# Kernel tuning notes

Hardware: AMD Instinct MI355X
Metric: run time of the kernel (lower is better)

## Reference

```python
import jax, jax.numpy as jnp
import numpy as np

N, F, H, L, O, E = 20000, 128, 128, 4, 64, 640000
NEG_SLOPE = 0.2  # PyG GATConv default


def setup_inputs() -> dict:
    key = jax.random.key(0)
    ks = jax.random.split(key, 8)
    x = jax.random.normal(ks[0], (N, F), dtype=jnp.float32)
    edge_index = jax.random.randint(ks[1], (2, E), 0, N, dtype=jnp.int64)
    sc = 1.0 / np.sqrt(F)
    Ws = jax.random.normal(ks[2], (L, F, H), dtype=jnp.float32) * sc
    att_src = jax.random.normal(ks[3], (L, H), dtype=jnp.float32) * sc
    att_dst = jax.random.normal(ks[4], (L, H), dtype=jnp.float32) * sc
    biases = jnp.zeros((L, H), dtype=jnp.float32)
    W_out = jax.random.normal(ks[5], (H, O), dtype=jnp.float32) * (1.0 / np.sqrt(H))
    b_out = jnp.zeros((O,), dtype=jnp.float32)
    return {"x": x, "edge_index": edge_index, "Ws": Ws, "att_src": att_src,
            "att_dst": att_dst, "biases": biases, "W_out": W_out, "b_out": b_out}


def _gat_conv(h, src, dst, W, a_s, a_d, b):
    # h: [N, F_in]; single-head GATConv (PyG semantics)
    z = h @ W                                   # [N, H]
    alpha_s = z @ a_s                           # [N]
    alpha_d = z @ a_d                           # [N]
    logits = jax.nn.leaky_relu(alpha_s[src] + alpha_d[dst], negative_slope=NEG_SLOPE)  # [E']
    # segment-softmax over edges grouped by destination node
    m = jax.ops.segment_max(logits, dst, num_segments=N)
    p = jnp.exp(logits - m[dst])
    s = jax.ops.segment_sum(p, dst, num_segments=N)
    alpha = p / (s[dst] + 1e-16)                # [E']
    out = jax.ops.segment_sum(alpha[:, None] * z[src], dst, num_segments=N)  # [N, H]
    return out + b


def reference(x, edge_index, Ws, att_src, att_dst, biases, W_out, b_out):
    # add self-loops once (PyG GATConv default add_self_loops=True)
    loop = jnp.arange(N, dtype=edge_index.dtype)
    src = jnp.concatenate([edge_index[0], loop])
    dst = jnp.concatenate([edge_index[1], loop])
    h = x
    for l in range(L):
        h = _gat_conv(h, src, dst, Ws[l], att_src[l], att_dst[l], biases[l])
        h = jax.nn.relu(h)  # Dropout is identity at eval
    return h @ W_out + b_out  # [N, O]
```

## Files before the change

kernel.cpp:

```cpp
#include <hip/hip_runtime.h>

#define NN 20000
#define FF 128
#define HH 128
#define LL 4
#define OO 64
#define EE 640000
#define NEG 0.2f
#define NB ((NN + 255) / 256)
#define NTILES (NN / 16)
#define ZS 132

typedef short bf16x8 __attribute__((ext_vector_type(8)));
typedef float f32x4 __attribute__((ext_vector_type(4)));

__device__ inline ushort f2bf(float f) {
    uint u = __float_as_uint(f);
    return (ushort)((u + 0x7fffu + ((u >> 16) & 1u)) >> 16);
}


__global__ void k_init_counters(int* __restrict__ counters) {
    int i = blockIdx.x * 256 + threadIdx.x;
    if (i < NN) counters[i] = 1;
}

__global__ void k_hist(const int* __restrict__ dst, int* __restrict__ counters) {
    int e = blockIdx.x * 256 + threadIdx.x;
    if (e < EE) atomicAdd(&counters[dst[e]], 1);
}

__global__ void k_partial(const int* __restrict__ counters, int* __restrict__ partials) {
    __shared__ int ws[4];
    int t = threadIdx.x;
    int i = blockIdx.x * 256 + t;
    int c = (i < NN) ? counters[i] : 0;
    #pragma unroll
    for (int off = 32; off; off >>= 1) c += __shfl_xor(c, off);
    if ((t & 63) == 0) ws[t >> 6] = c;
    __syncthreads();
    if (t == 0) partials[blockIdx.x] = ws[0] + ws[1] + ws[2] + ws[3];
}

__global__ void k_scan_small(const int* __restrict__ partials, int* __restrict__ offsets) {
    __shared__ int sp[128];
    int t = threadIdx.x;
    int v = (t < NB) ? partials[t] : 0;
    sp[t] = v;
    __syncthreads();
    for (int off = 1; off < 128; off <<= 1) {
        int u = (t >= off) ? sp[t - off] : 0;
        __syncthreads();
        sp[t] += u;
        __syncthreads();
    }
    if (t < NB) offsets[t] = sp[t] - v;
}

__global__ void k_apply(const int* __restrict__ counters, const int* __restrict__ offsets,
                        int* __restrict__ row_off, int* __restrict__ cursor,
                        int* __restrict__ src_sorted) {
    __shared__ int sc[256];
    int t = threadIdx.x;
    int i = blockIdx.x * 256 + t;
    int c = (i < NN) ? counters[i] : 0;
    sc[t] = c;
    __syncthreads();
    for (int off = 1; off < 256; off <<= 1) {
        int u = (t >= off) ? sc[t - off] : 0;
        __syncthreads();
        sc[t] += u;
        __syncthreads();
    }
    int incl = sc[t];
    int base = offsets[blockIdx.x];
    if (i < NN) {
        int excl = base + incl - c;
        row_off[i] = excl;
        cursor[i] = excl + 1;
        src_sorted[excl] = i;
        if (i == NN - 1) row_off[NN] = base + incl;
    }
}

__global__ void k_scatter(const int* __restrict__ src, const int* __restrict__ dst,
                          int* __restrict__ cursor, int* __restrict__ src_sorted) {
    int e = blockIdx.x * 256 + threadIdx.x;
    if (e < EE) {
        int p = atomicAdd(&cursor[dst[e]], 1);
        src_sorted[p] = src[e];
    }
}


__global__ void k_convw(const float* __restrict__ Ws, const float* __restrict__ Wout,
                        ushort* __restrict__ wh, ushort* __restrict__ wl) {
    int idx = blockIdx.x * 256 + threadIdx.x;
    const int per_l = HH * 128;
    float v;
    if (idx < LL * per_l) {
        int l = idx / per_l, rem = idx % per_l;
        int n = rem >> 7, k = rem & 127;
        v = Ws[(size_t)l * 128 * HH + (size_t)k * HH + n];
    } else {
        int j = idx - LL * per_l;
        if (j >= OO * 128) return;
        int n = j >> 7, k = j & 127;
        v = Wout[(size_t)k * OO + n];
    }
    ushort h = f2bf(v);
    float hf = __uint_as_float((uint)h << 16);
    wh[idx] = h;
    wl[idx] = f2bf(v - hf);
}


__global__ void k_wa(const float* __restrict__ Ws, const float* __restrict__ attS,
                     const float* __restrict__ attD, float* __restrict__ wa) {
    int t = blockIdx.x * 256 + threadIdx.x;
    if (t >= LL * 256) return;
    int l = t >> 8, rem = t & 255, which = rem >> 7, k = rem & 127;
    const float* wrow = Ws + (size_t)l * 128 * HH + (size_t)k * HH;
    const float* av = (which ? attD : attS) + l * HH;
    float s = 0.f;
    #pragma unroll 4
    for (int n = 0; n < HH; n++) s += wrow[n] * av[n];
    wa[l * 256 + which * 128 + k] = s;
}


__device__ inline void do_agg(const float* __restrict__ zin, const int* __restrict__ row_off,
                              const int* __restrict__ srcs, const float* __restrict__ bias,
                              float (*h)[132], int node0, int wid, int l64) {
    int g = l64 >> 5, cl = l64 & 31;
    const float4* zb = (const float4*)zin;
    #pragma unroll 1
    for (int i = 0; i < 2; i++) {
        int node = node0 + wid * 2 + i;
        int beg = row_off[node], end = row_off[node + 1];
        float adn = zin[(size_t)node * ZS + 1];
        float lself = zin[(size_t)node * ZS] + adn;
        float mx = (lself >= 0.f) ? lself : NEG * lself;

        float4 acc = make_float4(0.f, 0.f, 0.f, 0.f);
        float s = 0.f;
        for (int e = beg + g; e < end; e += 16) {
            int e1 = e + 2, e2 = e + 4, e3 = e + 6, e4 = e + 8, e5 = e + 10, e6 = e + 12, e7 = e + 14;
            int lim = end - 1;
            int i1 = min(e1, lim), i2 = min(e2, lim), i3 = min(e3, lim);
            int i4 = min(e4, lim), i5 = min(e5, lim), i6 = min(e6, lim), i7 = min(e7, lim);
            int s0 = srcs[e], s1 = srcs[i1], s2 = srcs[i2], s3 = srcs[i3];
            int s4 = srcs[i4], s5 = srcs[i5], s6 = srcs[i6], s7 = srcs[i7];
            float l0 = zin[(size_t)s0 * ZS] + adn, l1 = zin[(size_t)s1 * ZS] + adn;
            float l2 = zin[(size_t)s2 * ZS] + adn, l3 = zin[(size_t)s3 * ZS] + adn;
            float l4 = zin[(size_t)s4 * ZS] + adn, l5 = zin[(size_t)s5 * ZS] + adn;
            float l6 = zin[(size_t)s6 * ZS] + adn, l7 = zin[(size_t)s7 * ZS] + adn;
            l0 = (l0 >= 0.f) ? l0 : NEG * l0;  l1 = (l1 >= 0.f) ? l1 : NEG * l1;
            l2 = (l2 >= 0.f) ? l2 : NEG * l2;  l3 = (l3 >= 0.f) ? l3 : NEG * l3;
            l4 = (l4 >= 0.f) ? l4 : NEG * l4;  l5 = (l5 >= 0.f) ? l5 : NEG * l5;
            l6 = (l6 >= 0.f) ? l6 : NEG * l6;  l7 = (l7 >= 0.f) ? l7 : NEG * l7;
            float4 z0 = zb[(size_t)s0 * 33 + 1 + cl];
            float4 z1 = zb[(size_t)s1 * 33 + 1 + cl];
            float4 z2 = zb[(size_t)s2 * 33 + 1 + cl];
            float4 z3 = zb[(size_t)s3 * 33 + 1 + cl];
            float4 z4 = zb[(size_t)s4 * 33 + 1 + cl];
            float4 z5 = zb[(size_t)s5 * 33 + 1 + cl];
            float4 z6 = zb[(size_t)s6 * 33 + 1 + cl];
            float4 z7 = zb[(size_t)s7 * 33 + 1 + cl];
            float p0 = __expf(l0 - mx);
            float p1 = (e1 < end) ? __expf(l1 - mx) : 0.f;
            float p2 = (e2 < end) ? __expf(l2 - mx) : 0.f;
            float p3 = (e3 < end) ? __expf(l3 - mx) : 0.f;
            float p4 = (e4 < end) ? __expf(l4 - mx) : 0.f;
            float p5 = (e5 < end) ? __expf(l5 - mx) : 0.f;
            float p6 = (e6 < end) ? __expf(l6 - mx) : 0.f;
            float p7 = (e7 < end) ? __expf(l7 - mx) : 0.f;
            s += ((p0 + p1) + (p2 + p3)) + ((p4 + p5) + (p6 + p7));
            acc.x += (p0 * z0.x + p1 * z1.x + p2 * z2.x + p3 * z3.x)
                   + (p4 * z4.x + p5 * z5.x + p6 * z6.x + p7 * z7.x);
            acc.y += (p0 * z0.y + p1 * z1.y + p2 * z2.y + p3 * z3.y)
                   + (p4 * z4.y + p5 * z5.y + p6 * z6.y + p7 * z7.y);
            acc.z += (p0 * z0.z + p1 * z1.z + p2 * z2.z + p3 * z3.z)
                   + (p4 * z4.z + p5 * z5.z + p6 * z6.z + p7 * z7.z);
            acc.w += (p0 * z0.w + p1 * z1.w + p2 * z2.w + p3 * z3.w)
                   + (p4 * z4.w + p5 * z5.w + p6 * z6.w + p7 * z7.w);
        }
        acc.x += __shfl_xor(acc.x, 32);
        acc.y += __shfl_xor(acc.y, 32);
        acc.z += __shfl_xor(acc.z, 32);
        acc.w += __shfl_xor(acc.w, 32);
        s     += __shfl_xor(s, 32);
        if (g == 0) {
            float inv = 1.f / (s + 1e-16f);
            float4 b = ((const float4*)bias)[cl];
            int lrow = wid * 2 + i;
            h[lrow][cl * 4 + 0] = fmaxf(acc.x * inv + b.x, 0.f);
            h[lrow][cl * 4 + 1] = fmaxf(acc.y * inv + b.y, 0.f);
            h[lrow][cl * 4 + 2] = fmaxf(acc.z * inv + b.z, 0.f);
            h[lrow][cl * 4 + 3] = fmaxf(acc.w * inv + b.w, 0.f);
        }
    }
}

template <int NCOL, bool BIAS, bool ALPHAS, bool PACKED>
__device__ inline void do_gemm(const float (*h)[132], const ushort* __restrict__ wh,
                               const ushort* __restrict__ wl, const float* __restrict__ bias,
                               float* __restrict__ C, const float* __restrict__ wa,
                               int row0, int wid, int l64) {
    constexpr int CT = NCOL / 16;
    if (wid >= CT) return;
    int lr = l64 & 15, lg = l64 >> 4;
    int col0 = wid * 16;

    f32x4 af0[4], af1[4];
    #pragma unroll
    for (int s = 0; s < 4; s++) {
        af0[s] = *(const f32x4*)&h[lr][s * 32 + lg * 8];
        af1[s] = *(const f32x4*)&h[lr][s * 32 + lg * 8 + 4];
    }
    bf16x8 ah[4], al[4];
    #pragma unroll
    for (int s = 0; s < 4; s++) {
        #pragma unroll
        for (int j = 0; j < 8; j++) {
            float v = (j < 4) ? af0[s][j] : af1[s][j - 4];
            ushort hb = f2bf(v);
            float hf = __uint_as_float((uint)hb << 16);
            ah[s][j] = (short)hb;
            al[s][j] = (short)f2bf(v - hf);
        }
    }

    f32x4 acc = {0.f, 0.f, 0.f, 0.f};
    #pragma unroll
    for (int s = 0; s < 4; s++) {
        int woff = (col0 + lr) * 128 + s * 32 + lg * 8;
        bf16x8 bh = *(const bf16x8*)(wh + woff);
        bf16x8 bl = *(const bf16x8*)(wl + woff);
        acc = __builtin_amdgcn_mfma_f32_16x16x32_bf16(ah[s], bh, acc, 0, 0, 0);
        acc = __builtin_amdgcn_mfma_f32_16x16x32_bf16(ah[s], bl, acc, 0, 0, 0);
        acc = __builtin_amdgcn_mfma_f32_16x16x32_bf16(al[s], bh, acc, 0, 0, 0);
    }

    int orow = lg * 4;
    #pragma unroll
    for (int r = 0; r < 4; r++) {
        float v = acc[r];
        if (BIAS) v += bias[col0 + lr];
        if (PACKED)
            C[(size_t)(row0 + orow + r) * ZS + 4 + col0 + lr] = v;
        else
            C[(size_t)(row0 + orow + r) * NCOL + col0 + lr] = v;
    }

    if constexpr (ALPHAS) {
        if (wid == 0) {
            float ps = 0.f, pd = 0.f;
            #pragma unroll
            for (int s = 0; s < 4; s++) {
                #pragma unroll
                for (int j = 0; j < 8; j++) {
                    float v = (j < 4) ? af0[s][j] : af1[s][j - 4];
                    int k = s * 32 + lg * 8 + j;
                    ps += v * wa[k];
                    pd += v * wa[128 + k];
                }
            }
            ps += __shfl_xor(ps, 16);  pd += __shfl_xor(pd, 16);
            ps += __shfl_xor(ps, 32);  pd += __shfl_xor(pd, 32);
            if (lg == 0) {
                C[(size_t)(row0 + lr) * ZS + 0] = ps;
                C[(size_t)(row0 + lr) * ZS + 1] = pd;
            }
        }
    }
}


__global__ __launch_bounds__(512)
void k_layer0(const float* __restrict__ x, const ushort* __restrict__ wh,
              const ushort* __restrict__ wl, const float* __restrict__ wa,
              float* __restrict__ z) {
    __shared__ float h[16][132];
    int t = threadIdx.x, wid = t >> 6, l64 = t & 63;
    int row0 = blockIdx.x * 16;
    {
        int r = t >> 5, c4 = (t & 31) << 2;
        *(float4*)&h[r][c4] = *(const float4*)&x[(size_t)(row0 + r) * 128 + c4];
    }
    __syncthreads();
    do_gemm<HH, false, true, true>(h, wh, wl, nullptr, z, wa, row0, wid, l64);
}

template <int NCOL, bool BIAS, bool ALPHAS, bool PACKED>
__global__ __launch_bounds__(512)
void k_layer(const float* __restrict__ zin, const int* __restrict__ row_off,
             const int* __restrict__ srcs, const float* __restrict__ abias,
             const ushort* __restrict__ wh, const ushort* __restrict__ wl,
             const float* __restrict__ cbias, const float* __restrict__ wa,
             float* __restrict__ zout) {
    __shared__ float h[16][132];
    int t = threadIdx.x, wid = t >> 6, l64 = t & 63;
    int row0 = blockIdx.x * 16;
    do_agg(zin, row_off, srcs, abias, h, row0, wid, l64);
    __syncthreads();
    do_gemm<NCOL, BIAS, ALPHAS, PACKED>(h, wh, wl, cbias, zout, wa, row0, wid, l64);
}


extern "C" void kernel_launch(void* const* d_in, const int* in_sizes, int n_in,
                              void* d_out, int out_size, void* d_ws, size_t ws_size,
                              hipStream_t stream) {
    const float* x      = (const float*)d_in[0];
    const int*   ei     = (const int*)d_in[1];
    const float* Ws     = (const float*)d_in[2];
    const float* attS   = (const float*)d_in[3];
    const float* attD   = (const float*)d_in[4];
    const float* biases = (const float*)d_in[5];
    const float* W_out  = (const float*)d_in[6];
    const float* b_out  = (const float*)d_in[7];
    float* out = (float*)d_out;

    const int* srcp = ei;
    const int* dstp = ei + EE;

    char* w = (char*)d_ws;
    auto take = [&](size_t bytes) {
        char* p = w;
        w += (bytes + 15) & ~(size_t)15;
        return p;
    };
    float*  za         = (float*)take((size_t)NN * ZS * 4);
    float*  zbv        = (float*)take((size_t)NN * ZS * 4);
    int*    counters   = (int*)take((size_t)NN * 4);
    int*    row_off    = (int*)take((size_t)(NN + 1) * 4);
    int*    cursor     = (int*)take((size_t)NN * 4);
    int*    src_sorted = (int*)take((size_t)(EE + NN) * 4);
    int*    partials   = (int*)take((size_t)NB * 4);
    int*    offsets    = (int*)take((size_t)NB * 4);
    const int WTOT = LL * HH * 128 + OO * 128;
    ushort* whbuf      = (ushort*)take((size_t)WTOT * 2);
    ushort* wlbuf      = (ushort*)take((size_t)WTOT * 2);
    float*  wabuf      = (float*)take((size_t)LL * 256 * 4);

    k_init_counters<<<(NN + 255) / 256, 256, 0, stream>>>(counters);
    k_hist<<<(EE + 255) / 256, 256, 0, stream>>>(dstp, counters);
    k_partial<<<NB, 256, 0, stream>>>(counters, partials);
    k_scan_small<<<1, 128, 0, stream>>>(partials, offsets);
    k_apply<<<NB, 256, 0, stream>>>(counters, offsets, row_off, cursor, src_sorted);
    k_scatter<<<(EE + 255) / 256, 256, 0, stream>>>(srcp, dstp, cursor, src_sorted);
    k_convw<<<(WTOT + 255) / 256, 256, 0, stream>>>(Ws, W_out, whbuf, wlbuf);
    k_wa<<<(LL * 256 + 255) / 256, 256, 0, stream>>>(Ws, attS, attD, wabuf);

    k_layer0<<<NTILES, 512, 0, stream>>>(x, whbuf, wlbuf, wabuf, za);

    k_layer<HH, false, true, true><<<NTILES, 512, 0, stream>>>(
        za, row_off, src_sorted, biases + 0 * HH,
        whbuf + (size_t)1 * HH * 128, wlbuf + (size_t)1 * HH * 128,
        nullptr, wabuf + 1 * 256, zbv);
    k_layer<HH, false, true, true><<<NTILES, 512, 0, stream>>>(
        zbv, row_off, src_sorted, biases + 1 * HH,
        whbuf + (size_t)2 * HH * 128, wlbuf + (size_t)2 * HH * 128,
        nullptr, wabuf + 2 * 256, za);
    k_layer<HH, false, true, true><<<NTILES, 512, 0, stream>>>(
        za, row_off, src_sorted, biases + 2 * HH,
        whbuf + (size_t)3 * HH * 128, wlbuf + (size_t)3 * HH * 128,
        nullptr, wabuf + 3 * 256, zbv);

    k_layer<OO, true, false, false><<<NTILES, 512, 0, stream>>>(
        zbv, row_off, src_sorted, biases + 3 * HH,
        whbuf + (size_t)LL * HH * 128, wlbuf + (size_t)LL * HH * 128,
        b_out, nullptr, out);
}
```

Before: 361.0 us.

## Split node features into column-quarter planes and separate attention scalar arrays

Stores the per-node feature matrix as four 32-column planes of size NN×32, and moves the source and destination attention scalars into their own dense arrays. The aggregation now loops over the four planes, with 8 lanes covering 32 columns and 8 edge groups per wave. The goal is for each 128B gathered row segment to be reused from a smaller cache working set. The cost is that the edge list and source indices are re-read four times per node, each pass has less unrolling to overlap memory latency, and more shuffle reductions are needed.

```diff
diff --git a/kernel.cpp b/kernel.cpp
--- a/kernel.cpp
+++ b/kernel.cpp
@@ -9,7 +9,6 @@
 #define NEG 0.2f
 #define NB ((NN + 255) / 256)
 #define NTILES (NN / 16)
-#define ZS 132
 
 typedef short bf16x8 __attribute__((ext_vector_type(8)));
 typedef float f32x4 __attribute__((ext_vector_type(4)));
@@ -129,83 +128,77 @@
 }
 
 
-__device__ inline void do_agg(const float* __restrict__ zin, const int* __restrict__ row_off,
+__device__ inline void do_agg(const float* __restrict__ zq, const float* __restrict__ asv,
+                              const float* __restrict__ adv, const int* __restrict__ row_off,
                               const int* __restrict__ srcs, const float* __restrict__ bias,
                               float (*h)[132], int node0, int wid, int l64) {
-    int g = l64 >> 5, cl = l64 & 31;
-    const float4* zb = (const float4*)zin;
+    int c4 = l64 & 7, ep = l64 >> 3;
     #pragma unroll 1
     for (int i = 0; i < 2; i++) {
         int node = node0 + wid * 2 + i;
         int beg = row_off[node], end = row_off[node + 1];
-        float adn = zin[(size_t)node * ZS + 1];
-        float lself = zin[(size_t)node * ZS] + adn;
+        float adn = adv[node];
+        float lself = asv[node] + adn;
         float mx = (lself >= 0.f) ? lself : NEG * lself;
-
-        float4 acc = make_float4(0.f, 0.f, 0.f, 0.f);
-        float s = 0.f;
-        for (int e = beg + g; e < end; e += 16) {
-            int e1 = e + 2, e2 = e + 4, e3 = e + 6, e4 = e + 8, e5 = e + 10, e6 = e + 12, e7 = e + 14;
-            int lim = end - 1;
-            int i1 = min(e1, lim), i2 = min(e2, lim), i3 = min(e3, lim);
-            int i4 = min(e4, lim), i5 = min(e5, lim), i6 = min(e6, lim), i7 = min(e7, lim);
-            int s0 = srcs[e], s1 = srcs[i1], s2 = srcs[i2], s3 = srcs[i3];
-            int s4 = srcs[i4], s5 = srcs[i5], s6 = srcs[i6], s7 = srcs[i7];
-            float l0 = zin[(size_t)s0 * ZS] + adn, l1 = zin[(size_t)s1 * ZS] + adn;
-            float l2 = zin[(size_t)s2 * ZS] + adn, l3 = zin[(size_t)s3 * ZS] + adn;
-            float l4 = zin[(size_t)s4 * ZS] + adn, l5 = zin[(size_t)s5 * ZS] + adn;
-            float l6 = zin[(size_t)s6 * ZS] + adn, l7 = zin[(size_t)s7 * ZS] + adn;
-            l0 = (l0 >= 0.f) ? l0 : NEG * l0;  l1 = (l1 >= 0.f) ? l1 : NEG * l1;
-            l2 = (l2 >= 0.f) ? l2 : NEG * l2;  l3 = (l3 >= 0.f) ? l3 : NEG * l3;
-            l4 = (l4 >= 0.f) ? l4 : NEG * l4;  l5 = (l5 >= 0.f) ? l5 : NEG * l5;
-            l6 = (l6 >= 0.f) ? l6 : NEG * l6;  l7 = (l7 >= 0.f) ? l7 : NEG * l7;
-            float4 z0 = zb[(size_t)s0 * 33 + 1 + cl];
-            float4 z1 = zb[(size_t)s1 * 33 + 1 + cl];
-            float4 z2 = zb[(size_t)s2 * 33 + 1 + cl];
-            float4 z3 = zb[(size_t)s3 * 33 + 1 + cl];
-            float4 z4 = zb[(size_t)s4 * 33 + 1 + cl];
-            float4 z5 = zb[(size_t)s5 * 33 + 1 + cl];
-            float4 z6 = zb[(size_t)s6 * 33 + 1 + cl];
-            float4 z7 = zb[(size_t)s7 * 33 + 1 + cl];
-            float p0 = __expf(l0 - mx);
-            float p1 = (e1 < end) ? __expf(l1 - mx) : 0.f;
-            float p2 = (e2 < end) ? __expf(l2 - mx) : 0.f;
-            float p3 = (e3 < end) ? __expf(l3 - mx) : 0.f;
-            float p4 = (e4 < end) ? __expf(l4 - mx) : 0.f;
-            float p5 = (e5 < end) ? __expf(l5 - mx) : 0.f;
-            float p6 = (e6 < end) ? __expf(l6 - mx) : 0.f;
-            float p7 = (e7 < end) ? __expf(l7 - mx) : 0.f;
-            s += ((p0 + p1) + (p2 + p3)) + ((p4 + p5) + (p6 + p7));
-            acc.x += (p0 * z0.x + p1 * z1.x + p2 * z2.x + p3 * z3.x)
-                   + (p4 * z4.x + p5 * z5.x + p6 * z6.x + p7 * z7.x);
-            acc.y += (p0 * z0.y + p1 * z1.y + p2 * z2.y + p3 * z3.y)
-                   + (p4 * z4.y + p5 * z5.y + p6 * z6.y + p7 * z7.y);
-            acc.z += (p0 * z0.z + p1 * z1.z + p2 * z2.z + p3 * z3.z)
-                   + (p4 * z4.z + p5 * z5.z + p6 * z6.z + p7 * z7.z);
-            acc.w += (p0 * z0.w + p1 * z1.w + p2 * z2.w + p3 * z3.w)
-                   + (p4 * z4.w + p5 * z5.w + p6 * z6.w + p7 * z7.w);
+        int lrow = wid * 2 + i;
+
+        #pragma unroll 1
+        for (int q = 0; q < 4; q++) {
+            const float* qbase = zq + (size_t)q * NN * 32;
+            float4 acc = make_float4(0.f, 0.f, 0.f, 0.f);
+            float s = 0.f;
+            for (int e = beg + ep; e < end; e += 16) {
+                int lim = end - 1;
+                int i1 = min(e + 8, lim);
+                int s0 = srcs[e], s1 = srcs[i1];
+                float l0 = asv[s0] + adn, l1 = asv[s1] + adn;
+                l0 = (l0 >= 0.f) ? l0 : NEG * l0;
+                l1 = (l1 >= 0.f) ? l1 : NEG * l1;
+                float4 z0 = *(const float4*)(qbase + (size_t)s0 * 32 + c4 * 4);
+                float4 z1 = *(const float4*)(qbase + (size_t)s1 * 32 + c4 * 4);
+                float p0 = __expf(l0 - mx);
+                float p1 = (e + 8 < end) ? __expf(l1 - mx) : 0.f;
+                s += p0 + p1;
+                acc.x += p0 * z0.x + p1 * z1.x;
+                acc.y += p0 * z0.y + p1 * z1.y;
+                acc.z += p0 * z0.z + p1 * z1.z;
+                acc.w += p0 * z0.w + p1 * z1.w;
+            }
+            acc.x += __shfl_xor(acc.x, 8);
+            acc.y += __shfl_xor(acc.y, 8);
+            acc.z += __shfl_xor(acc.z, 8);
+            acc.w += __shfl_xor(acc.w, 8);
+            s     += __shfl_xor(s, 8);
+            acc.x += __shfl_xor(acc.x, 16);
+            acc.y += __shfl_xor(acc.y, 16);
+            acc.z += __shfl_xor(acc.z, 16);
+            acc.w += __shfl_xor(acc.w, 16);
+            s     += __shfl_xor(s, 16);
+            acc.x += __shfl_xor(acc.x, 32);
+            acc.y += __shfl_xor(acc.y, 32);
+            acc.z += __shfl_xor(acc.z, 32);
+            acc.w += __shfl_xor(acc.w, 32);
+            s     += __shfl_xor(s, 32);
+            if (ep == 0) {
+                float inv = 1.f / (s + 1e-16f);
+                float4 b = ((const float4*)bias)[q * 8 + c4];
+                float4 o;
+                o.x = fmaxf(acc.x * inv + b.x, 0.f);
+                o.y = fmaxf(acc.y * inv + b.y, 0.f);
+                o.z = fmaxf(acc.z * inv + b.z, 0.f);
+                o.w = fmaxf(acc.w * inv + b.w, 0.f);
+                *(float4*)&h[lrow][q * 32 + c4 * 4] = o;
+            }
         }
-        acc.x += __shfl_xor(acc.x, 32);
-        acc.y += __shfl_xor(acc.y, 32);
-        acc.z += __shfl_xor(acc.z, 32);
-        acc.w += __shfl_xor(acc.w, 32);
-        s     += __shfl_xor(s, 32);
-        if (g == 0) {
-            float inv = 1.f / (s + 1e-16f);
-            float4 b = ((const float4*)bias)[cl];
-            int lrow = wid * 2 + i;
-            h[lrow][cl * 4 + 0] = fmaxf(acc.x * inv + b.x, 0.f);
-            h[lrow][cl * 4 + 1] = fmaxf(acc.y * inv + b.y, 0.f);
-            h[lrow][cl * 4 + 2] = fmaxf(acc.z * inv + b.z, 0.f);
-            h[lrow][cl * 4 + 3] = fmaxf(acc.w * inv + b.w, 0.f);
-        }
-    }
-}
+    }
+}
+
 
 template <int NCOL, bool BIAS, bool ALPHAS, bool PACKED>
 __device__ inline void do_gemm(const float (*h)[132], const ushort* __restrict__ wh,
                                const ushort* __restrict__ wl, const float* __restrict__ bias,
                                float* __restrict__ C, const float* __restrict__ wa,
+                               float* __restrict__ as_o, float* __restrict__ ad_o,
                                int row0, int wid, int l64) {
     constexpr int CT = NCOL / 16;
     if (wid >= CT) return;
@@ -243,14 +236,15 @@
     }
 
     int orow = lg * 4;
+    int c = col0 + lr;
     #pragma unroll
     for (int r = 0; r < 4; r++) {
         float v = acc[r];
-        if (BIAS) v += bias[col0 + lr];
+        if (BIAS) v += bias[c];
         if (PACKED)
-            C[(size_t)(row0 + orow + r) * ZS + 4 + col0 + lr] = v;
+            C[((size_t)(c >> 5) * NN + (row0 + orow + r)) * 32 + (c & 31)] = v;
         else
-            C[(size_t)(row0 + orow + r) * NCOL + col0 + lr] = v;
+            C[(size_t)(row0 + orow + r) * NCOL + c] = v;
     }
 
     if constexpr (ALPHAS) {
@@ -269,8 +263,8 @@
             ps += __shfl_xor(ps, 16);  pd += __shfl_xor(pd, 16);
             ps += __shfl_xor(ps, 32);  pd += __shfl_xor(pd, 32);
             if (lg == 0) {
-                C[(size_t)(row0 + lr) * ZS + 0] = ps;
-                C[(size_t)(row0 + lr) * ZS + 1] = pd;
+                as_o[row0 + lr] = ps;
+                ad_o[row0 + lr] = pd;
             }
         }
     }
@@ -280,7 +274,7 @@
 __global__ __launch_bounds__(512)
 void k_layer0(const float* __restrict__ x, const ushort* __restrict__ wh,
               const ushort* __restrict__ wl, const float* __restrict__ wa,
-              float* __restrict__ z) {
+              float* __restrict__ zq, float* __restrict__ as_o, float* __restrict__ ad_o) {
     __shared__ float h[16][132];
     int t = threadIdx.x, wid = t >> 6, l64 = t & 63;
     int row0 = blockIdx.x * 16;
@@ -289,22 +283,24 @@
         *(float4*)&h[r][c4] = *(const float4*)&x[(size_t)(row0 + r) * 128 + c4];
     }
     __syncthreads();
-    do_gemm<HH, false, true, true>(h, wh, wl, nullptr, z, wa, row0, wid, l64);
+    do_gemm<HH, false, true, true>(h, wh, wl, nullptr, zq, wa, as_o, ad_o, row0, wid, l64);
 }
 
 template <int NCOL, bool BIAS, bool ALPHAS, bool PACKED>
 __global__ __launch_bounds__(512)
-void k_layer(const float* __restrict__ zin, const int* __restrict__ row_off,
+void k_layer(const float* __restrict__ zin, const float* __restrict__ asi,
+             const float* __restrict__ adi, const int* __restrict__ row_off,
              const int* __restrict__ srcs, const float* __restrict__ abias,
              const ushort* __restrict__ wh, const ushort* __restrict__ wl,
              const float* __restrict__ cbias, const float* __restrict__ wa,
-             float* __restrict__ zout) {
+             float* __restrict__ zout, float* __restrict__ as_o, float* __restrict__ ad_o) {
     __shared__ float h[16][132];
     int t = threadIdx.x, wid = t >> 6, l64 = t & 63;
     int row0 = blockIdx.x * 16;
-    do_agg(zin, row_off, srcs, abias, h, row0, wid, l64);
-    __syncthreads();
-    do_gemm<NCOL, BIAS, ALPHAS, PACKED>(h, wh, wl, cbias, zout, wa, row0, wid, l64);
+    do_agg(zin, asi, adi, row_off, srcs, abias, h, row0, wid, l64);
+    __syncthreads();
+    do_gemm<NCOL, BIAS, ALPHAS, PACKED>(h, wh, wl, cbias, zout, wa, as_o, ad_o,
+                                        row0, wid, l64);
 }
 
 
@@ -330,8 +326,12 @@
         w += (bytes + 15) & ~(size_t)15;
         return p;
     };
-    float*  za         = (float*)take((size_t)NN * ZS * 4);
-    float*  zbv        = (float*)take((size_t)NN * ZS * 4);
+    float*  zqa        = (float*)take((size_t)NN * 128 * 4);
+    float*  zqb        = (float*)take((size_t)NN * 128 * 4);
+    float*  asa        = (float*)take((size_t)NN * 4);
+    float*  ada        = (float*)take((size_t)NN * 4);
+    float*  asb        = (float*)take((size_t)NN * 4);
+    float*  adb        = (float*)take((size_t)NN * 4);
     int*    counters   = (int*)take((size_t)NN * 4);
     int*    row_off    = (int*)take((size_t)(NN + 1) * 4);
     int*    cursor     = (int*)take((size_t)NN * 4);
@@ -352,23 +352,23 @@
     k_convw<<<(WTOT + 255) / 256, 256, 0, stream>>>(Ws, W_out, whbuf, wlbuf);
     k_wa<<<(LL * 256 + 255) / 256, 256, 0, stream>>>(Ws, attS, attD, wabuf);
 
-    k_layer0<<<NTILES, 512, 0, stream>>>(x, whbuf, wlbuf, wabuf, za);
+    k_layer0<<<NTILES, 512, 0, stream>>>(x, whbuf, wlbuf, wabuf, zqa, asa, ada);
 
     k_layer<HH, false, true, true><<<NTILES, 512, 0, stream>>>(
-        za, row_off, src_sorted, biases + 0 * HH,
+        zqa, asa, ada, row_off, src_sorted, biases + 0 * HH,
         whbuf + (size_t)1 * HH * 128, wlbuf + (size_t)1 * HH * 128,
-        nullptr, wabuf + 1 * 256, zbv);
+        nullptr, wabuf + 1 * 256, zqb, asb, adb);
     k_layer<HH, false, true, true><<<NTILES, 512, 0, stream>>>(
-        zbv, row_off, src_sorted, biases + 1 * HH,
+        zqb, asb, adb, row_off, src_sorted, biases + 1 * HH,
         whbuf + (size_t)2 * HH * 128, wlbuf + (size_t)2 * HH * 128,
-        nullptr, wabuf + 2 * 256, za);
+        nullptr, wabuf + 2 * 256, zqa, asa, ada);
     k_layer<HH, false, true, true><<<NTILES, 512, 0, stream>>>(
-        za, row_off, src_sorted, biases + 2 * HH,
+        zqa, asa, ada, row_off, src_sorted, biases + 2 * HH,
         whbuf + (size_t)3 * HH * 128, wlbuf + (size_t)3 * HH * 128,
-        nullptr, wabuf + 3 * 256, zbv);
+        nullptr, wabuf + 3 * 256, zqb, asb, adb);
 
     k_layer<OO, true, false, false><<<NTILES, 512, 0, stream>>>(
-        zbv, row_off, src_sorted, biases + 3 * HH,
+        zqb, asb, adb, row_off, src_sorted, biases + 3 * HH,
         whbuf + (size_t)LL * HH * 128, wlbuf + (size_t)LL * HH * 128,
-        b_out, nullptr, out);
-}
+        b_out, nullptr, out, nullptr, nullptr);
+}
```

New measurement: 459.4 us. +27.3%, slower.
